# Kernel tuning notes

Measured on AMD Instinct MI355X. Metric: run time of the kernel, lower is better.

The kernel has to match this reference:

```python
import jax, jax.numpy as jnp
import numpy as np

B, S, D, H = 16, 512, 1024, 16
DH = D // H  # 64


def setup_inputs() -> dict:
    key = jax.random.key(0)
    kx, kq, kk, kv = jax.random.split(key, 4)
    stdv = 1.0 / np.sqrt(DH)  # reset_param uses 1/sqrt(t.size(1)) = 1/sqrt(head_dim)
    x = jax.random.normal(kx, (B, S, D), dtype=jnp.float32)
    Wq = jax.random.uniform(kq, (H, D, DH), dtype=jnp.float32, minval=-stdv, maxval=stdv)
    Wk = jax.random.uniform(kk, (H, D, DH), dtype=jnp.float32, minval=-stdv, maxval=stdv)
    Wv = jax.random.uniform(kv, (H, D, DH), dtype=jnp.float32, minval=-stdv, maxval=stdv)
    return {"x": x, "Wq": Wq, "Wk": Wk, "Wv": Wv}


def reference(x, Wq, Wk, Wv):
    # x: [B, S, D]; Wq/Wk/Wv: [H, D, DH] (stacked per-head params)
    q = jnp.einsum('bsd,hde->bhse', x, Wq)  # [B,H,S,DH]
    k = jnp.einsum('bsd,hde->bhse', x, Wk)
    v = jnp.einsum('bsd,hde->bhse', x, Wv)
    # NOTE: original scales by sqrt(input_dim), not sqrt(head_dim)
    scale = 1.0 / jnp.sqrt(jnp.float32(D))
    scores = jnp.einsum('bhse,bhte->bhst', q, k) * scale  # [B,H,S,S]
    attn = jax.nn.softmax(scores, axis=-1)
    out = jnp.einsum('bhst,bhte->bhse', attn, v)  # [B,H,S,DH]
    # concat heads along feature dim (head order matches torch cat over loop)
    return out.transpose(0, 2, 1, 3).reshape(x.shape[0], x.shape[1], D)
```

## Files before the change

kernel.cpp:

```cpp
#include <hip/hip_runtime.h>
#include <math.h>

constexpr int B = 16, S = 512, D = 1024, H = 16, DH = 64;
constexpr int BH = B * H;

typedef short bf16x8 __attribute__((ext_vector_type(8)));
typedef float f32x4  __attribute__((ext_vector_type(4)));
typedef float f32x16 __attribute__((ext_vector_type(16)));

__device__ __forceinline__ unsigned short f2bf(float f) {
    unsigned u = __float_as_uint(f);
    u += 0x7fff + ((u >> 16) & 1);
    return (unsigned short)(u >> 16);
}

#define VMC0  asm volatile("s_waitcnt vmcnt(0)" ::: "memory")
#define LGKM0 asm volatile("s_waitcnt lgkmcnt(0)" ::: "memory")
#define BARR  __builtin_amdgcn_s_barrier()

__global__ __launch_bounds__(256) void convert_all(
    const float* __restrict__ x, unsigned short* __restrict__ xb,
    const float* __restrict__ Wq, const float* __restrict__ Wk,
    const float* __restrict__ Wv, unsigned short* __restrict__ WbT)
{
    __shared__ float tile[64][65];
    const int t = threadIdx.x;
    const int bx = blockIdx.x;

    if (bx < 8192) {
        int i = bx * 256 + t;
        float4 v = ((const float4*)x)[i];
        ushort4 o;
        o.x = f2bf(v.x); o.y = f2bf(v.y); o.z = f2bf(v.z); o.w = f2bf(v.w);
        ((ushort4*)xb)[i] = o;
        return;
    }

    const int cw = bx - 8192;
    const int d0 = (cw & 15) * 64;
    const int h = (cw >> 4) & 15;
    const int m = cw >> 8;
    const float* W = ((m == 0) ? Wq : (m == 1) ? Wk : Wv) + (size_t)h * D * DH;
    {
        int e = t & 63, dr = t >> 6;
        #pragma unroll
        for (int i = 0; i < 16; ++i) {
            int d = dr * 16 + i;
            tile[d][e] = W[(size_t)(d0 + d) * DH + e];
        }
    }
    __syncthreads();
    {
        int d = t & 63, er = t >> 6;
        unsigned short* out = WbT + (size_t)(m * H + h) * DH * D;
        #pragma unroll
        for (int i = 0; i < 16; ++i) {
            int e = er * 16 + i;
            out[(size_t)e * D + d0 + d] = f2bf(tile[d][e]);
        }
    }
}

__global__ __launch_bounds__(256) void qkv_gemm(
    const unsigned short* __restrict__ xb,
    const unsigned short* __restrict__ WbT,
    unsigned short* __restrict__ qkvb, int n_base)
{
    __shared__ unsigned short As[128 * 64];
    __shared__ unsigned short Bs[128 * 64];

    const int t = threadIdx.x;
    const int w = t >> 6;
    const int wr = w >> 1, wc = w & 1;
    const int L = t & 63;
    const int lane31 = L & 31;
    const int hi = L >> 5;
    const int lrow8 = L >> 3;
    const int lg = L & 7;

    const int r0 = blockIdx.x * 128;
    const int n0 = n_base + blockIdx.y * 128;

    f32x16 acc[2][2] = {};

    for (int k0 = 0; k0 < D; k0 += 64) {
        #pragma unroll
        for (int i = 0; i < 4; ++i) {
            int c = w * 4 + i;
            int r = c * 8 + lrow8;
            int gg = lg ^ (r & 7);
            const unsigned short* gp = xb + (size_t)(r0 + r) * D + k0 + gg * 8;
            __builtin_amdgcn_global_load_lds(
                (const __attribute__((address_space(1))) void*)gp,
                (__attribute__((address_space(3))) void*)(As + c * 512),
                16, 0, 0);
            const unsigned short* gq = WbT + (size_t)(n0 + r) * D + k0 + gg * 8;
            __builtin_amdgcn_global_load_lds(
                (const __attribute__((address_space(1))) void*)gq,
                (__attribute__((address_space(3))) void*)(Bs + c * 512),
                16, 0, 0);
        }
        __syncthreads();

        #pragma unroll
        for (int ks4 = 0; ks4 < 4; ++ks4) {
            int g = ks4 * 2 + hi;
            bf16x8 a[2], bb[2];
            #pragma unroll
            for (int rt = 0; rt < 2; ++rt) {
                int ml = wr * 64 + rt * 32 + lane31;
                a[rt] = *(const bf16x8*)(As + ml * 64 + ((g ^ (ml & 7)) * 8));
            }
            #pragma unroll
            for (int ct = 0; ct < 2; ++ct) {
                int nl = wc * 64 + ct * 32 + lane31;
                bb[ct] = *(const bf16x8*)(Bs + nl * 64 + ((g ^ (nl & 7)) * 8));
            }
            #pragma unroll
            for (int rt = 0; rt < 2; ++rt)
                #pragma unroll
                for (int ct = 0; ct < 2; ++ct)
                    acc[rt][ct] = __builtin_amdgcn_mfma_f32_32x32x16_bf16(
                        a[rt], bb[ct], acc[rt][ct], 0, 0, 0);
        }
        __syncthreads();
    }

    const int m  = n0 >> 10;
    const int h  = ((n0 >> 6) + wc) & 15;
    const int bb_ = r0 >> 9;
    const int s0 = (r0 & 511) + wr * 64;

    if (m == 2) {
        unsigned short* outv = qkvb + ((size_t)(2 * BH) + (bb_ * H + h)) * (size_t)(S * DH);
        #pragma unroll
        for (int rt = 0; rt < 2; ++rt)
            #pragma unroll
            for (int ct = 0; ct < 2; ++ct) {
                int e = ct * 32 + lane31;
                #pragma unroll
                for (int rg = 0; rg < 4; ++rg) {
                    int srow = s0 + rt * 32 + rg * 8 + hi * 4;
                    ushort4 pk;
                    pk.x = f2bf(acc[rt][ct][rg * 4 + 0]);
                    pk.y = f2bf(acc[rt][ct][rg * 4 + 1]);
                    pk.z = f2bf(acc[rt][ct][rg * 4 + 2]);
                    pk.w = f2bf(acc[rt][ct][rg * 4 + 3]);
                    *(ushort4*)(outv + (size_t)e * S + srow) = pk;
                }
            }
    } else {
        const float sc = (m == 0) ? 0.04508422002778011f : 1.0f;
        unsigned short* out = qkvb + ((size_t)m * BH + (bb_ * H + h)) * (size_t)(S * DH);
        #pragma unroll
        for (int rt = 0; rt < 2; ++rt)
            #pragma unroll
            for (int ct = 0; ct < 2; ++ct) {
                int e = ct * 32 + lane31;
                #pragma unroll
                for (int r = 0; r < 16; ++r) {
                    int srow = s0 + rt * 32 + (r & 3) + 8 * (r >> 2) + 4 * hi;
                    out[(size_t)srow * DH + e] = f2bf(acc[rt][ct][r] * sc);
                }
            }
    }
}

__global__ __launch_bounds__(512, 4) void attn_mfma(
    const unsigned short* __restrict__ qkvb, float* __restrict__ out)
{
    __shared__ unsigned short KV[2][2][64 * 64];
    unsigned short* Qs = &KV[0][0][0];

    const int t = threadIdx.x;
    const int w = t >> 6;
    const int L = t & 63;
    const int lane15 = L & 15;
    const int quad = L >> 4;
    const int lrow8 = L >> 3;
    const int lg = L & 7;
    const int qr0 = blockIdx.x * 128;
    const int bh = blockIdx.y;
    const int b = bh >> 4, h = bh & 15;

    const unsigned short* qb = qkvb + (size_t)bh * S * DH;
    const unsigned short* kb = qkvb + (size_t)(BH + bh) * S * DH;
    const unsigned short* vt = qkvb + (size_t)(2 * BH + bh) * S * DH;

    #pragma unroll
    for (int p = 0; p < 2; ++p) {
        int base = p * 64 + w * 8;
        int r = base + lrow8;
        int gg = lg ^ (r & 7);
        __builtin_amdgcn_global_load_lds(
            (const __attribute__((address_space(1))) void*)
                (qb + (size_t)(qr0 + r) * DH + gg * 8),
            (__attribute__((address_space(3))) void*)(Qs + base * 64),
            16, 0, 0);
    }
    VMC0;
    BARR;

    bf16x8 qf[2];
    #pragma unroll
    for (int ks = 0; ks < 2; ++ks) {
        int ml = w * 16 + lane15;
        int gk = ks * 4 + quad;
        qf[ks] = *(const bf16x8*)(Qs + ml * 64 + ((gk ^ (lane15 & 7)) * 8));
    }
    LGKM0;
    BARR;

    {
        int r = w * 8 + lrow8;
        int gr = (r & 32) | ((r & 12) << 1) | ((r & 16) >> 2) | (r & 3);
        int gg = lg ^ (r & 7);
        __builtin_amdgcn_global_load_lds(
            (const __attribute__((address_space(1))) void*)
                (kb + (size_t)gr * DH + gg * 8),
            (__attribute__((address_space(3))) void*)(&KV[0][0][0] + (w * 8) * 64),
            16, 0, 0);
        __builtin_amdgcn_global_load_lds(
            (const __attribute__((address_space(1))) void*)
                (vt + (size_t)r * S + gg * 8),
            (__attribute__((address_space(3))) void*)(&KV[0][1][0] + (w * 8) * 64),
            16, 0, 0);
    }
    VMC0;
    BARR;

    f32x4 o[4] = {};
    float plsum = 0.f;

    #pragma unroll 2
    for (int kt = 0; kt < 8; ++kt) {
        const int cur = kt & 1;
        const unsigned short* Kt  = &KV[cur][0][0];
        const unsigned short* Vtl = &KV[cur][1][0];

        f32x4 st[4] = {};
        #pragma unroll
        for (int ks = 0; ks < 2; ++ks) {
            int gk = ks * 4 + quad;
            bf16x8 kf[4];
            #pragma unroll
            for (int ct = 0; ct < 4; ++ct) {
                int kr = ct * 16 + lane15;
                kf[ct] = *(const bf16x8*)(Kt + kr * 64 + ((gk ^ (lane15 & 7)) * 8));
            }
            __builtin_amdgcn_s_setprio(1);
            #pragma unroll
            for (int ct = 0; ct < 4; ++ct)
                st[ct] = __builtin_amdgcn_mfma_f32_16x16x32_bf16(
                    kf[ct], qf[ks], st[ct], 0, 0, 0);
            __builtin_amdgcn_s_setprio(0);
        }

        bf16x8 pB[2];
        {
            float rs = 0.f;
            union { unsigned u[4]; bf16x8 v; } pu[2];
            #pragma unroll
            for (int ct = 0; ct < 4; ++ct) {
                float p0 = exp2f(st[ct][0]);
                float p1 = exp2f(st[ct][1]);
                float p2 = exp2f(st[ct][2]);
                float p3 = exp2f(st[ct][3]);
                rs += (p0 + p1) + (p2 + p3);
                unsigned lo, hi;
                asm("v_cvt_pk_bf16_f32 %0, %1, %2" : "=v"(lo) : "v"(p0), "v"(p1));
                asm("v_cvt_pk_bf16_f32 %0, %1, %2" : "=v"(hi) : "v"(p2), "v"(p3));
                pu[ct >> 1].u[(ct & 1) * 2 + 0] = lo;
                pu[ct >> 1].u[(ct & 1) * 2 + 1] = hi;
            }
            pB[0] = pu[0].v;
            pB[1] = pu[1].v;
            plsum += rs;
        }

        #pragma unroll
        for (int ks = 0; ks < 2; ++ks) {
            int gk = ks * 4 + quad;
            bf16x8 vf[4];
            #pragma unroll
            for (int nt = 0; nt < 4; ++nt) {
                int dh = nt * 16 + lane15;
                vf[nt] = *(const bf16x8*)(Vtl + dh * 64 + ((gk ^ (lane15 & 7)) * 8));
            }
            __builtin_amdgcn_s_setprio(1);
            #pragma unroll
            for (int nt = 0; nt < 4; ++nt)
                o[nt] = __builtin_amdgcn_mfma_f32_16x16x32_bf16(
                    vf[nt], pB[ks], o[nt], 0, 0, 0);
            __builtin_amdgcn_s_setprio(0);
        }

        if (kt < 7) {
            int r = w * 8 + lrow8;
            int gr = (r & 32) | ((r & 12) << 1) | ((r & 16) >> 2) | (r & 3);
            int gg = lg ^ (r & 7);
            int kn = (kt + 1) * 64;
            __builtin_amdgcn_global_load_lds(
                (const __attribute__((address_space(1))) void*)
                    (kb + (size_t)(kn + gr) * DH + gg * 8),
                (__attribute__((address_space(3))) void*)(&KV[cur ^ 1][0][0] + (w * 8) * 64),
                16, 0, 0);
            __builtin_amdgcn_global_load_lds(
                (const __attribute__((address_space(1))) void*)
                    (vt + (size_t)r * S + kn + gg * 8),
                (__attribute__((address_space(3))) void*)(&KV[cur ^ 1][1][0] + (w * 8) * 64),
                16, 0, 0);
            VMC0;
            BARR;
        }
    }

    {
        float l = plsum;
        l += __shfl_xor(l, 16, 64);
        l += __shfl_xor(l, 32, 64);
        float inv = 1.0f / l;
        int srow = qr0 + w * 16 + lane15;
        float* op = out + (size_t)(b * S + srow) * D + h * DH;
        #pragma unroll
        for (int nt = 0; nt < 4; ++nt) {
            float4 v;
            v.x = o[nt][0] * inv;
            v.y = o[nt][1] * inv;
            v.z = o[nt][2] * inv;
            v.w = o[nt][3] * inv;
            *(float4*)(op + nt * 16 + quad * 4) = v;
        }
    }
}

extern "C" void kernel_launch(void* const* d_in, const int* in_sizes, int n_in,
                              void* d_out, int out_size, void* d_ws, size_t ws_size,
                              hipStream_t stream) {
    const float* x  = (const float*)d_in[0];
    const float* Wq = (const float*)d_in[1];
    const float* Wk = (const float*)d_in[2];
    const float* Wv = (const float*)d_in[3];
    float* outp = (float*)d_out;

    unsigned short* qkvb = (unsigned short*)d_ws;
    unsigned short* xb   = (unsigned short*)((char*)d_ws + 50331648);
    unsigned short* WbT  = (unsigned short*)((char*)d_ws + 67108864);

    convert_all<<<dim3(8192 + 768), 256, 0, stream>>>(x, xb, Wq, Wk, Wv, WbT);
    qkv_gemm<<<dim3(B * S / 128, 16), 256, 0, stream>>>(xb, WbT, qkvb, 0);
    qkv_gemm<<<dim3(B * S / 128, 8),  256, 0, stream>>>(xb, WbT, qkvb, 2048);
    attn_mfma<<<dim3(S / 128, BH), 512, 0, stream>>>(qkvb, outp);
}
```

Before: 197.3 us.

## Double-buffer QKV GEMM LDS tiles and merge two launches into one

The QKV projection GEMM now uses two LDS buffers. The next K-slice is prefetched with global_load_lds while MFMAs run on the current slice, and all fragment reads are hoisted ahead of the MFMA chain with raised wave priority. The two separate qkv_gemm launches (Q/K and V) are merged into a single 64x24 grid. This hides global load latency behind compute and removes one launch, at the cost of doubled LDS use (64 KB per block), which may reduce occupancy, and more registers held for fragments.

```diff
diff --git a/kernel.cpp b/kernel.cpp
--- a/kernel.cpp
+++ b/kernel.cpp
@@ -61,13 +61,37 @@
     }
 }
 
+__device__ __forceinline__ void qkv_stage(
+    const unsigned short* __restrict__ xb,
+    const unsigned short* __restrict__ WbT,
+    unsigned short* Ad, unsigned short* Bd,
+    int r0, int n0, int k0, int w, int lrow8, int lg)
+{
+    #pragma unroll
+    for (int i = 0; i < 4; ++i) {
+        int c = w * 4 + i;
+        int r = c * 8 + lrow8;
+        int gg = lg ^ (r & 7);
+        __builtin_amdgcn_global_load_lds(
+            (const __attribute__((address_space(1))) void*)
+                (xb + (size_t)(r0 + r) * D + k0 + gg * 8),
+            (__attribute__((address_space(3))) void*)(Ad + c * 512),
+            16, 0, 0);
+        __builtin_amdgcn_global_load_lds(
+            (const __attribute__((address_space(1))) void*)
+                (WbT + (size_t)(n0 + r) * D + k0 + gg * 8),
+            (__attribute__((address_space(3))) void*)(Bd + c * 512),
+            16, 0, 0);
+    }
+}
+
 __global__ __launch_bounds__(256) void qkv_gemm(
     const unsigned short* __restrict__ xb,
     const unsigned short* __restrict__ WbT,
-    unsigned short* __restrict__ qkvb, int n_base)
+    unsigned short* __restrict__ qkvb)
 {
-    __shared__ unsigned short As[128 * 64];
-    __shared__ unsigned short Bs[128 * 64];
+    __shared__ unsigned short As[2][128 * 64];
+    __shared__ unsigned short Bs[2][128 * 64];
 
     const int t = threadIdx.x;
     const int w = t >> 6;
@@ -79,51 +103,52 @@
     const int lg = L & 7;
 
     const int r0 = blockIdx.x * 128;
-    const int n0 = n_base + blockIdx.y * 128;
+    const int n0 = blockIdx.y * 128;
 
     f32x16 acc[2][2] = {};
 
-    for (int k0 = 0; k0 < D; k0 += 64) {
-        #pragma unroll
-        for (int i = 0; i < 4; ++i) {
-            int c = w * 4 + i;
-            int r = c * 8 + lrow8;
-            int gg = lg ^ (r & 7);
-            const unsigned short* gp = xb + (size_t)(r0 + r) * D + k0 + gg * 8;
-            __builtin_amdgcn_global_load_lds(
-                (const __attribute__((address_space(1))) void*)gp,
-                (__attribute__((address_space(3))) void*)(As + c * 512),
-                16, 0, 0);
-            const unsigned short* gq = WbT + (size_t)(n0 + r) * D + k0 + gg * 8;
-            __builtin_amdgcn_global_load_lds(
-                (const __attribute__((address_space(1))) void*)gq,
-                (__attribute__((address_space(3))) void*)(Bs + c * 512),
-                16, 0, 0);
-        }
-        __syncthreads();
-
+    qkv_stage(xb, WbT, &As[0][0], &Bs[0][0], r0, n0, 0, w, lrow8, lg);
+    VMC0;
+    BARR;
+
+    #pragma unroll 2
+    for (int kt = 0; kt < 16; ++kt) {
+        const int cur = kt & 1;
+
+        bf16x8 a[4][2], bb[4][2];
         #pragma unroll
         for (int ks4 = 0; ks4 < 4; ++ks4) {
             int g = ks4 * 2 + hi;
-            bf16x8 a[2], bb[2];
             #pragma unroll
             for (int rt = 0; rt < 2; ++rt) {
                 int ml = wr * 64 + rt * 32 + lane31;
-                a[rt] = *(const bf16x8*)(As + ml * 64 + ((g ^ (ml & 7)) * 8));
+                a[ks4][rt] = *(const bf16x8*)(&As[cur][0] + ml * 64 + ((g ^ (ml & 7)) * 8));
             }
             #pragma unroll
             for (int ct = 0; ct < 2; ++ct) {
                 int nl = wc * 64 + ct * 32 + lane31;
-                bb[ct] = *(const bf16x8*)(Bs + nl * 64 + ((g ^ (nl & 7)) * 8));
-            }
+                bb[ks4][ct] = *(const bf16x8*)(&Bs[cur][0] + nl * 64 + ((g ^ (nl & 7)) * 8));
+            }
+        }
+        __builtin_amdgcn_sched_barrier(0);
+
+        if (kt < 15)
+            qkv_stage(xb, WbT, &As[cur ^ 1][0], &Bs[cur ^ 1][0],
+                      r0, n0, (kt + 1) * 64, w, lrow8, lg);
+
+        __builtin_amdgcn_s_setprio(1);
+        #pragma unroll
+        for (int ks4 = 0; ks4 < 4; ++ks4)
             #pragma unroll
             for (int rt = 0; rt < 2; ++rt)
                 #pragma unroll
                 for (int ct = 0; ct < 2; ++ct)
                     acc[rt][ct] = __builtin_amdgcn_mfma_f32_32x32x16_bf16(
-                        a[rt], bb[ct], acc[rt][ct], 0, 0, 0);
-        }
-        __syncthreads();
+                        a[ks4][rt], bb[ks4][ct], acc[rt][ct], 0, 0, 0);
+        __builtin_amdgcn_s_setprio(0);
+
+        VMC0;
+        BARR;
     }
 
     const int m  = n0 >> 10;
@@ -348,7 +373,6 @@
     unsigned short* WbT  = (unsigned short*)((char*)d_ws + 67108864);
 
     convert_all<<<dim3(8192 + 768), 256, 0, stream>>>(x, xb, Wq, Wk, Wv, WbT);
-    qkv_gemm<<<dim3(B * S / 128, 16), 256, 0, stream>>>(xb, WbT, qkvb, 0);
-    qkv_gemm<<<dim3(B * S / 128, 8),  256, 0, stream>>>(xb, WbT, qkvb, 2048);
+    qkv_gemm<<<dim3(B * S / 128, 3 * H * DH / 128), 256, 0, stream>>>(xb, WbT, qkvb);
     attn_mfma<<<dim3(S / 128, BH), 512, 0, stream>>>(qkvb, outp);
 }
```

Measured after the change: 186.7 us. -5.4%, faster.
